# Performance work log

Hardware: AMD Instinct MI355X
Metric: run time of the kernel (lower is better)

The kernel has to match this reference:

```python
import jax, jax.numpy as jnp
import numpy as np

CP_LEN = 256
FFT_SIZE = 1024
OFFSET = CP_LEN // 2                      # 128
PILOT_SPACING = 100
NSYMS = 824
TOTAL_SYMS = NSYMS + 1 + NSYMS // PILOT_SPACING   # 833
PAD_L = (FFT_SIZE - TOTAL_SYMS) // 2      # 95
PAD_R = FFT_SIZE - PAD_L - TOTAL_SYMS     # 96
PILOTS_IDX = np.arange(PAD_L, FFT_SIZE - PAD_R, PILOT_SPACING)  # 9 pilots

def _data_indices():
    # Statically unroll the original while-loop: gather all non-pilot data bins.
    idxs = []
    idx = 0
    jj = PAD_L + 1
    while idx < NSYMS:
        n = min(PILOT_SPACING - 1, NSYMS - idx)
        idxs.extend(range(jj, jj + n))
        idx += n
        jj += n + 1
    return np.asarray(idxs, dtype=np.int32)

DATA_IDX = _data_indices()  # [824]


def setup_inputs() -> dict:
    key = jax.random.key(0)
    # [batch, n_symbols, 2*(FFT_SIZE+CP_LEN)] interleaved I/Q floats
    in1 = jax.random.normal(key, (16, 1024, 2 * (FFT_SIZE + CP_LEN)), dtype=jnp.float32)
    return {"in1": in1}


def reference(in1):
    t = jnp.arange(FFT_SIZE, dtype=jnp.float32)
    # Deinterleave I/Q -> complex64
    iq = jax.lax.complex(in1[:, :, ::2], in1[:, :, 1::2])
    # FFT of the window starting at half the CP, then fftshift via roll
    spec = jnp.fft.fft(iq[:, :, OFFSET:OFFSET + FFT_SIZE], axis=2)
    result = jnp.roll(spec, FFT_SIZE // 2, axis=2)
    # Compensate timing-offset phase ramp
    result = result * jnp.exp(1j * OFFSET * t * (2.0 * np.pi / FFT_SIZE))
    # Estimate residual slope from pilot phase differences (wrapped to [-pi,pi])
    a = jnp.diff(jnp.angle(result[:, :, PILOTS_IDX]), axis=2)
    a = jnp.where(a > np.pi, a - 2.0 * np.pi, a)
    a = jnp.where(a < -np.pi, a + 2.0 * np.pi, a)
    mn = jnp.mean(a, axis=2)  # [B, S]
    result = result * jnp.exp(-1j * t * mn[:, :, None] / PILOT_SPACING)
    # Gather data (non-pilot) bins and interleave real/imag -> [B, S, 2*NSYMS]
    data = result[:, :, DATA_IDX]
    x = jnp.stack([data.real, data.imag], axis=-1).reshape(
        data.shape[0], data.shape[1], 2 * NSYMS)
    return x.astype(jnp.float32)
```

## Files before the change

### kernel.cpp

```cpp
#include <hip/hip_runtime.h>
#include <math.h>

#define NT      256
#define NSYMS   824
#define NPILOT  9

#define PADIDX(k) ((k) + ((k) >> 4))

#define C32_TWOPI_1024  6.1359233222901821136474609375e-3f

__device__ __forceinline__ float2 cmulf(float2 a, float2 b) {
    return make_float2(a.x * b.x - a.y * b.y, a.x * b.y + a.y * b.x);
}

template <int T2>
__device__ __forceinline__ void r4_stage(const float2* __restrict__ src,
                                         float2* __restrict__ dst,
                                         const float2* __restrict__ W,
                                         int i) {
    const int s = 1 << T2;
    const int r = i & (s - 1);
    const int p = i & ~(s - 1);
    const int pb = PADIDX(i);
    float2 a = src[pb];
    float2 b = src[pb + 272];
    float2 c = src[pb + 544];
    float2 d = src[pb + 816];
    float2 w1 = W[PADIDX(p)];
    float2 w2 = W[PADIDX(2 * p)];
    float2 w3 = W[PADIDX(3 * p)];
    float2 t0  = make_float2(a.x + c.x, a.y + c.y);
    float2 t1  = make_float2(a.x - c.x, a.y - c.y);
    float2 t2c = make_float2(b.x + d.x, b.y + d.y);
    float2 t3  = make_float2(b.x - d.x, b.y - d.y);
    float2 y0  = make_float2(t0.x + t2c.x, t0.y + t2c.y);
    float2 e1  = make_float2(t1.x + t3.y, t1.y - t3.x);
    float2 e2  = make_float2(t0.x - t2c.x, t0.y - t2c.y);
    float2 e3  = make_float2(t1.x - t3.y, t1.y + t3.x);
    const int j0 = ((i >> T2) << (T2 + 2)) | r;
    dst[PADIDX(j0)]         = y0;
    dst[PADIDX(j0 + s)]     = cmulf(w1, e1);
    dst[PADIDX(j0 + 2 * s)] = cmulf(w2, e2);
    dst[PADIDX(j0 + 3 * s)] = cmulf(w3, e3);
}

__global__ __launch_bounds__(NT) void ofdm_kernel(const float* __restrict__ in,
                                                  float* __restrict__ out) {
    __shared__ float2  bufA[1088];
    __shared__ float2  bufB[1088];
    __shared__ float2  W[1088];
    __shared__ double2 T[1088];
    __shared__ double2 u_s[NT];
    __shared__ double2 pr[252];
    __shared__ double  ang[NPILOT];

    const int row = blockIdx.x;
    const int tid = threadIdx.x;

    const float2* rin2 = (const float2*)(in + (size_t)row * 2560) + 128;
    float2 v0 = rin2[tid];
    float2 v1 = rin2[tid + 256];
    float2 v2 = rin2[tid + 512];
    float2 v3 = rin2[tid + 768];

    double ux = ((double)v0.x - (double)v2.x) - ((double)v1.y - (double)v3.y);
    double uy = ((double)v0.y - (double)v2.y) + ((double)v1.x - (double)v3.x);

    {
        double sn, cs;
        sincos((double)tid * -6.1359231515425649189e-3, &sn, &cs);
        T[PADIDX(tid)]       = make_double2(cs, sn);
        T[PADIDX(tid + 256)] = make_double2(sn, -cs);
        T[PADIDX(tid + 512)] = make_double2(-cs, -sn);
        T[PADIDX(tid + 768)] = make_double2(-sn, cs);
        float cf = (float)cs, sf = (float)sn;
        W[PADIDX(tid)]       = make_float2(cf, sf);
        W[PADIDX(tid + 256)] = make_float2(sf, -cf);
        W[PADIDX(tid + 512)] = make_float2(-cf, -sf);
        W[PADIDX(tid + 768)] = make_float2(-sf, cf);
    }

    bufA[PADIDX(tid)]       = v0;
    bufA[PADIDX(tid + 256)] = v1;
    bufA[PADIDX(tid + 512)] = v2;
    bufA[PADIDX(tid + 768)] = v3;
    u_s[tid] = make_double2(ux, uy);
    __syncthreads();

    if (tid < 252) {
        int p = tid / 28;
        int g = tid - p * 28;
        int t0s = 10 * g;
        double2 acc = make_double2(0.0, 0.0);
        int nmax = 256 - t0s; if (nmax > 10) nmax = 10;
        if (nmax > 0) {
            int jj = 95 + 100 * p;
            int K = (jj + 512) & 1023;
            int idx = (K * t0s) & 1023;
            for (int m = 0; m < nmax; m++) {
                double2 w = T[PADIDX(idx)];
                double2 uu = u_s[t0s + m];
                acc.x += w.x * uu.x - w.y * uu.y;
                acc.y += w.x * uu.y + w.y * uu.x;
                idx = (idx + K) & 1023;
            }
        }
        pr[tid] = acc;
    }
    r4_stage<0>(bufA, bufB, W, tid);
    __syncthreads();

    if (tid < NPILOT) {
        double2 ssum = make_double2(0.0, 0.0);
        #pragma unroll
        for (int g = 0; g < 28; g++) {
            double2 q = pr[tid * 28 + g];
            ssum.x += q.x; ssum.y += q.y;
        }
        int jj = 95 + 100 * tid;
        float th32 = (float)(128 * jj) * C32_TWOPI_1024;
        double sn, cs;
        sincos((double)th32, &sn, &cs);
        double csf = (double)(float)cs;
        double snf = (double)(float)sn;
        double re = ssum.x * csf - ssum.y * snf;
        double im = ssum.x * snf + ssum.y * csf;
        ang[tid] = atan2(im, re);
    }
    r4_stage<2>(bufB, bufA, W, tid);
    __syncthreads();
    r4_stage<4>(bufA, bufB, W, tid);
    __syncthreads();
    r4_stage<6>(bufB, bufA, W, tid);
    __syncthreads();
    r4_stage<8>(bufA, bufB, W, tid);
    __syncthreads();

    double mn;
    {
        double sum = 0.0;
        double prev = ang[0];
        #pragma unroll
        for (int k = 1; k < NPILOT; k++) {
            double cur = ang[k];
            double a = cur - prev;
            if (a > 3.14159265358979323846)       a -= 6.28318530717958647693;
            else if (a < -3.14159265358979323846) a += 6.28318530717958647693;
            sum += a;
            prev = cur;
        }
        mn = sum * 0.125;
    }

    float2* rout = (float2*)(out + (size_t)row * (2 * NSYMS));
    #pragma unroll
    for (int jl = 0; jl < 4; jl++) {
        int d = tid + jl * NT;
        if (d < NSYMS) {
            int jj = 96 + d + d / 99;
            float2 z = bufB[PADIDX(jj ^ 512)];
            float th32 = (float)(128 * jj) * C32_TWOPI_1024;
            float ph = th32 - (float)(mn * 0.01 * (double)jj);
            float sn, cs;
            __sincosf(ph, &sn, &cs);
            rout[d] = make_float2(z.x * cs - z.y * sn,
                                  z.x * sn + z.y * cs);
        }
    }
}

extern "C" void kernel_launch(void* const* d_in, const int* in_sizes, int n_in,
                              void* d_out, int out_size, void* d_ws, size_t ws_size,
                              hipStream_t stream) {
    const float* in = (const float*)d_in[0];
    float* out = (float*)d_out;
    ofdm_kernel<<<dim3(16 * 1024), dim3(NT), 0, stream>>>(in, out);
}
```

Baseline: 320.2 us.

## Shrink LDS footprint, shuffle-reduce pilot DFT, fuse last FFT stage into output

The 1024-entry double twiddle table is replaced by a 256-entry quarter table with quadrant symmetry, and the unused last quarter of the float twiddles is dropped. This cuts shared memory per block, and launch bounds now request 5 waves per SIMD to raise occupancy. The pilot DFT now uses 16 lanes per pilot with a wave shuffle reduction instead of a shared partial-sum array, a second pass and a barrier. The final radix-4 stage is done in registers and written straight to the output, removing one LDS round trip and one barrier, at the cost of a more complex scattered data-bin index calculation.

```diff
diff --git a/kernel.cpp b/kernel.cpp
--- a/kernel.cpp
+++ b/kernel.cpp
@@ -44,14 +44,13 @@
     dst[PADIDX(j0 + 3 * s)] = cmulf(w3, e3);
 }
 
-__global__ __launch_bounds__(NT) void ofdm_kernel(const float* __restrict__ in,
-                                                  float* __restrict__ out) {
+__global__ __launch_bounds__(NT, 5) void ofdm_kernel(const float* __restrict__ in,
+                                                     float* __restrict__ out) {
+    __shared__ double2 T256[256];
+    __shared__ double2 u_s[NT];
     __shared__ float2  bufA[1088];
     __shared__ float2  bufB[1088];
-    __shared__ float2  W[1088];
-    __shared__ double2 T[1088];
-    __shared__ double2 u_s[NT];
-    __shared__ double2 pr[252];
+    __shared__ float2  W[816];
     __shared__ double  ang[NPILOT];
 
     const int row = blockIdx.x;
@@ -69,15 +68,11 @@
     {
         double sn, cs;
         sincos((double)tid * -6.1359231515425649189e-3, &sn, &cs);
-        T[PADIDX(tid)]       = make_double2(cs, sn);
-        T[PADIDX(tid + 256)] = make_double2(sn, -cs);
-        T[PADIDX(tid + 512)] = make_double2(-cs, -sn);
-        T[PADIDX(tid + 768)] = make_double2(-sn, cs);
+        T256[tid] = make_double2(cs, sn);
         float cf = (float)cs, sf = (float)sn;
         W[PADIDX(tid)]       = make_float2(cf, sf);
         W[PADIDX(tid + 256)] = make_float2(sf, -cf);
         W[PADIDX(tid + 512)] = make_float2(-cf, -sf);
-        W[PADIDX(tid + 768)] = make_float2(-sf, cf);
     }
 
     bufA[PADIDX(tid)]       = v0;
@@ -87,53 +82,49 @@
     u_s[tid] = make_double2(ux, uy);
     __syncthreads();
 
-    if (tid < 252) {
-        int p = tid / 28;
-        int g = tid - p * 28;
-        int t0s = 10 * g;
+    if (tid < 16 * NPILOT) {
+        const int p  = tid >> 4;
+        const int g  = tid & 15;
+        const int jj = 95 + 100 * p;
+        const int K  = (jj + 512) & 1023;
+        int idx = (K * g) & 1023;
+        const int step = (K * 16) & 1023;
         double2 acc = make_double2(0.0, 0.0);
-        int nmax = 256 - t0s; if (nmax > 10) nmax = 10;
-        if (nmax > 0) {
-            int jj = 95 + 100 * p;
-            int K = (jj + 512) & 1023;
-            int idx = (K * t0s) & 1023;
-            for (int m = 0; m < nmax; m++) {
-                double2 w = T[PADIDX(idx)];
-                double2 uu = u_s[t0s + m];
-                acc.x += w.x * uu.x - w.y * uu.y;
-                acc.y += w.x * uu.y + w.y * uu.x;
-                idx = (idx + K) & 1023;
-            }
+        #pragma unroll
+        for (int m = 0; m < 16; m++) {
+            double2 uu = u_s[g + 16 * m];
+            double2 w  = T256[idx & 255];
+            const int q = idx >> 8;
+            double wx = w.x, wy = w.y;
+            if (q & 1) { double t = wx; wx = wy; wy = -t; }
+            if (q & 2) { wx = -wx; wy = -wy; }
+            acc.x += wx * uu.x - wy * uu.y;
+            acc.y += wx * uu.y + wy * uu.x;
+            idx = (idx + step) & 1023;
         }
-        pr[tid] = acc;
+        #pragma unroll
+        for (int off = 1; off < 16; off <<= 1) {
+            acc.x += __shfl_xor(acc.x, off, 64);
+            acc.y += __shfl_xor(acc.y, off, 64);
+        }
+        if (g == 0) {
+            float th32 = (float)(128 * jj) * C32_TWOPI_1024;
+            double sn, cs;
+            sincos((double)th32, &sn, &cs);
+            double csf = (double)(float)cs;
+            double snf = (double)(float)sn;
+            double re = acc.x * csf - acc.y * snf;
+            double im = acc.x * snf + acc.y * csf;
+            ang[p] = atan2(im, re);
+        }
     }
     r4_stage<0>(bufA, bufB, W, tid);
     __syncthreads();
-
-    if (tid < NPILOT) {
-        double2 ssum = make_double2(0.0, 0.0);
-        #pragma unroll
-        for (int g = 0; g < 28; g++) {
-            double2 q = pr[tid * 28 + g];
-            ssum.x += q.x; ssum.y += q.y;
-        }
-        int jj = 95 + 100 * tid;
-        float th32 = (float)(128 * jj) * C32_TWOPI_1024;
-        double sn, cs;
-        sincos((double)th32, &sn, &cs);
-        double csf = (double)(float)cs;
-        double snf = (double)(float)sn;
-        double re = ssum.x * csf - ssum.y * snf;
-        double im = ssum.x * snf + ssum.y * csf;
-        ang[tid] = atan2(im, re);
-    }
     r4_stage<2>(bufB, bufA, W, tid);
     __syncthreads();
     r4_stage<4>(bufA, bufB, W, tid);
     __syncthreads();
     r4_stage<6>(bufB, bufA, W, tid);
-    __syncthreads();
-    r4_stage<8>(bufA, bufB, W, tid);
     __syncthreads();
 
     double mn;
@@ -152,19 +143,36 @@
         mn = sum * 0.125;
     }
 
-    float2* rout = (float2*)(out + (size_t)row * (2 * NSYMS));
-    #pragma unroll
-    for (int jl = 0; jl < 4; jl++) {
-        int d = tid + jl * NT;
-        if (d < NSYMS) {
-            int jj = 96 + d + d / 99;
-            float2 z = bufB[PADIDX(jj ^ 512)];
-            float th32 = (float)(128 * jj) * C32_TWOPI_1024;
-            float ph = th32 - (float)(mn * 0.01 * (double)jj);
-            float sn, cs;
-            __sincosf(ph, &sn, &cs);
-            rout[d] = make_float2(z.x * cs - z.y * sn,
-                                  z.x * sn + z.y * cs);
+    {
+        const int pb = PADIDX(tid);
+        float2 a = bufA[pb];
+        float2 b = bufA[pb + 272];
+        float2 c = bufA[pb + 544];
+        float2 d = bufA[pb + 816];
+        float2 t0  = make_float2(a.x + c.x, a.y + c.y);
+        float2 t1  = make_float2(a.x - c.x, a.y - c.y);
+        float2 t2c = make_float2(b.x + d.x, b.y + d.y);
+        float2 t3  = make_float2(b.x - d.x, b.y - d.y);
+        float2 y0  = make_float2(t0.x + t2c.x, t0.y + t2c.y);
+        float2 y1  = make_float2(t1.x + t3.y, t1.y - t3.x);
+        float2 y2  = make_float2(t0.x - t2c.x, t0.y - t2c.y);
+        float2 y3  = make_float2(t1.x - t3.y, t1.y + t3.x);
+
+        float2* rout = (float2*)(out + (size_t)row * (2 * NSYMS));
+        float2 ys[4] = { y2, y3, y0, y1 };
+        #pragma unroll
+        for (int k = 0; k < 4; k++) {
+            const int jj = tid + 256 * k;
+            if (jj >= 96 && jj <= 927 && ((jj - 95) % 100) != 0) {
+                const int dd = jj - 96 - (jj - 96) / 100;
+                float2 z = ys[k];
+                float th32 = (float)(128 * jj) * C32_TWOPI_1024;
+                float ph = th32 - (float)(mn * 0.01 * (double)jj);
+                float sn, cs;
+                __sincosf(ph, &sn, &cs);
+                rout[dd] = make_float2(z.x * cs - z.y * sn,
+                                       z.x * sn + z.y * cs);
+            }
         }
     }
 }
```

Result: faster. 294.6 us (-8.0%).
